# Kernel tuning notes

Hardware: AMD Instinct MI355X
Metric: run time of the kernel (lower is better)

Reference implementation:

```python
import jax, jax.numpy as jnp
import numpy as np

RADIUS = 0.07          # gno_config.gno_radius
SCALES = (1.0, 2.0)    # gno_config.scales


def _kernel_mlp(pair, kW1, kb1, kW2, kb2, kW3, kb3):
    # ChannelMLP inside IntegralTransform: gelu between layers, none after last
    h = jax.nn.gelu(pair @ kW1 + kb1)
    h = jax.nn.gelu(h @ kW2 + kb2)
    return h @ kW3 + kb3


def setup_inputs() -> dict:
    key = jax.random.key(0)
    ks = jax.random.split(key, 8)
    B, N, NL, CD, IN_C, C, H = 2, 2048, 512, 2, 16, 32, 32

    def glorot(k, shape):
        return jax.random.normal(k, shape) / jnp.sqrt(jnp.float32(shape[0]))

    return {
        "x_coord": jax.random.uniform(ks[0], (B, N, CD), dtype=jnp.float32),
        "pndata": jax.random.normal(ks[1], (B, N, IN_C), dtype=jnp.float32),
        "latent_tokens_coord": jax.random.uniform(ks[2], (NL, CD), dtype=jnp.float32),
        # lifting ChannelMLP (n_layers=1 -> single 1x1 conv == linear)
        "W_lift": glorot(ks[3], (IN_C, C)),
        "b_lift": jnp.zeros((C,), jnp.float32),
        # kernel MLP: [2*coord_dim=4] -> 32 -> 32 -> out_channels=32
        "kW1": glorot(ks[4], (2 * CD, H)),
        "kb1": jnp.zeros((H,), jnp.float32),
        "kW2": glorot(ks[5], (H, H)),
        "kb2": jnp.zeros((H,), jnp.float32),
        "kW3": glorot(ks[6], (H, C)),
        "kb3": jnp.zeros((C,), jnp.float32),
    }


def reference(x_coord, pndata, latent_tokens_coord,
              W_lift, b_lift, kW1, kb1, kW2, kb2, kW3, kb3):
    # lifting: [B,N,in_c] -> [B,N,C]
    f = pndata @ W_lift + b_lift

    B, N, CD = x_coord.shape
    NL = latent_tokens_coord.shape[0]

    y = x_coord[:, None, :, :]                      # [B,1,N,CD] source coords
    xq = latent_tokens_coord[None, :, None, :]      # [1,NL,1,CD] query coords
    # kernel input = cat(y_j, x_i) per (query i, source j) pair -> [B,NL,N,2*CD]
    pair = jnp.concatenate([jnp.broadcast_to(y, (B, NL, N, CD)),
                            jnp.broadcast_to(xq, (B, NL, N, CD))], axis=-1)
    kvals = _kernel_mlp(pair, kW1, kb1, kW2, kb2, kW3, kb3)  # [B,NL,N,C]

    d2 = jnp.sum((y - xq) ** 2, axis=-1)            # [B,NL,N] squared distances

    out = jnp.zeros((B, NL, kvals.shape[-1]), f.dtype)
    for s in SCALES:  # fixed small set of scales (2)
        # radius neighbor search expressed as dense mask (faithful to ball query)
        mask = (d2 <= (RADIUS * s) ** 2).astype(f.dtype)      # [B,NL,N]
        cnt = jnp.maximum(jnp.sum(mask, axis=-1), 1.0)        # [B,NL]
        # 'linear' transform: mean_j k(x_i,y_j) * f(y_j) over neighbors
        agg = jnp.einsum('bijc,bjc,bij->bic', kvals, f, mask)
        out = out + agg / cnt[..., None]
    return out  # [B,NL,C]
```

## Files before the change

kernel.cpp:

```cpp
#include <hip/hip_runtime.h>

static constexpr int B_ = 2, N_ = 2048, NL_ = 512, IN_C_ = 16, C_ = 32, H_ = 32;
static constexpr float R1SQ = (float)(0.07 * 0.07);
static constexpr float R2SQ = (float)(0.14 * 0.14);

typedef __attribute__((ext_vector_type(8))) short bf16x8;
typedef __attribute__((ext_vector_type(4))) float f32x4;

__device__ __forceinline__ float gelu_tanh(float x) {
    float z2 = 2.0f * 0.7978845608028654f * x * fmaf(0.044715f * x, x, 1.0f);
    float e = __expf(z2);
    return x * (1.0f - 1.0f / (e + 1.0f));
}

__device__ __forceinline__ short f2bf(float x) {
    unsigned u = __float_as_uint(x);
    u += 0x7fffu + ((u >> 16) & 1u);
    return (short)(u >> 16);
}

__global__ __launch_bounds__(128)
void magno_fused(const float* __restrict__ x_coord,
                 const float* __restrict__ lat,
                 const float* __restrict__ kW1, const float* __restrict__ kb1,
                 const float* __restrict__ kW2, const float* __restrict__ kb2,
                 const float* __restrict__ kW3, const float* __restrict__ kb3,
                 const float* __restrict__ pnd,
                 const float* __restrict__ Wl,
                 const float* __restrict__ bl,
                 float* __restrict__ out)
{
    __shared__ float sR0[H_], sR1[H_], sA1[H_];
    __shared__ unsigned jlist[N_];
    __shared__ __align__(16) short strans[2][64 * 40];
    __shared__ float sred[2][C_];
    __shared__ int s_n, s_c1;

    const int tid  = threadIdx.x;
    const int lane = tid & 63;
    const int wid  = tid >> 6;
    const int qd   = lane >> 4;
    const int li   = lane & 15;
    const int bi = blockIdx.x;
    const int b = bi >> 9, i = bi & (NL_ - 1);
    const float xq0 = lat[2 * i], xq1 = lat[2 * i + 1];

    if (tid == 0) { s_n = 0; s_c1 = 0; }
    if (tid < H_) {
        sR0[tid] = kW1[tid];
        sR1[tid] = kW1[H_ + tid];
        sA1[tid] = fmaf(xq0, kW1[2 * H_ + tid], fmaf(xq1, kW1[3 * H_ + tid], kb1[tid]));
    }

    bf16x8 w2f[2], w3f[2], wlf[2];
#pragma unroll
    for (int nt = 0; nt < 2; ++nt) {
        int n0 = li + 16 * nt;
#pragma unroll
        for (int jj = 0; jj < 8; ++jj) {
            int k = qd * 8 + jj;
            w2f[nt][jj] = f2bf(kW2[k * H_ + n0]);
            w3f[nt][jj] = f2bf(kW3[k * C_ + n0]);
            wlf[nt][jj] = (k < IN_C_) ? f2bf(Wl[k * C_ + n0]) : (short)0;
        }
    }
    const float b2A = kb2[li], b2B = kb2[li + 16];
    const float b3A = kb3[li], b3B = kb3[li + 16];
    const float blA = bl[li],  blB = bl[li + 16];
    __syncthreads();

    const float2* __restrict__ xc = (const float2*)(x_coord + (size_t)b * N_ * 2);
    const unsigned long long ltmask = (1ull << lane) - 1ull;
    for (int j0 = tid; j0 < N_; j0 += 128) {
        float2 y = xc[j0];
        float dy0 = y.x - xq0, dy1 = y.y - xq1;
        float d2 = dy0 * dy0 + dy1 * dy1;
        bool in2 = d2 <= R2SQ;
        bool in1 = d2 <= R1SQ;
        unsigned long long m2 = __ballot(in2);
        unsigned long long m1 = __ballot(in1);
        int basew = 0;
        if (lane == 0) {
            basew = atomicAdd(&s_n, __popcll(m2));
            atomicAdd(&s_c1, __popcll(m1));
        }
        basew = __shfl(basew, 0, 64);
        if (in2) {
            int pos = basew + __popcll(m2 & ltmask);
            jlist[pos] = (unsigned)j0 | (in1 ? 0x80000000u : 0u);
        }
    }
    __syncthreads();
    const int n = s_n;
    const float inv2 = 1.0f / (float)(n > 0 ? n : 1);
    const float inv1 = 1.0f / (float)(s_c1 > 0 ? s_c1 : 1);

    float r0v[8], r1v[8], a1v[8];
#pragma unroll
    for (int jj = 0; jj < 8; ++jj) {
        int k = qd * 8 + jj;
        r0v[jj] = sR0[k]; r1v[jj] = sR1[k]; a1v[jj] = sA1[k];
    }

    const float* __restrict__ pbase = pnd + (size_t)b * N_ * IN_C_;
    short* tb = &strans[wid][0];

    float accA = 0.0f, accB = 0.0f;
    const int nIter = (n + 127) >> 7;

    for (int it = 0; it < nIter; ++it) {
        const int base = it * 128 + 64 * wid;

        bf16x8 hfrag[4], paf[4];
#pragma unroll
        for (int mt = 0; mt < 4; ++mt) {
            int e = base + 16 * mt + li;
            unsigned pk = jlist[e < N_ ? e : 0];
            int j = (int)(pk & (unsigned)(N_ - 1));
            float2 y = xc[j];
#pragma unroll
            for (int jj = 0; jj < 8; ++jj)
                hfrag[mt][jj] = f2bf(gelu_tanh(fmaf(y.x, r0v[jj], fmaf(y.y, r1v[jj], a1v[jj]))));
            if (qd < 2) {
                const float4* p4 = (const float4*)(pbase + (size_t)j * IN_C_ + qd * 8);
                float4 v0 = p4[0], v1 = p4[1];
                paf[mt][0] = f2bf(v0.x); paf[mt][1] = f2bf(v0.y);
                paf[mt][2] = f2bf(v0.z); paf[mt][3] = f2bf(v0.w);
                paf[mt][4] = f2bf(v1.x); paf[mt][5] = f2bf(v1.y);
                paf[mt][6] = f2bf(v1.z); paf[mt][7] = f2bf(v1.w);
            } else {
#pragma unroll
                for (int jj = 0; jj < 8; ++jj) paf[mt][jj] = (short)0;
            }
        }

        f32x4 accF[4][2], acc2[4][2];
#pragma unroll
        for (int mt = 0; mt < 4; ++mt)
#pragma unroll
            for (int nt = 0; nt < 2; ++nt) {
                f32x4 z = {0.f, 0.f, 0.f, 0.f};
                accF[mt][nt] = __builtin_amdgcn_mfma_f32_16x16x32_bf16(paf[mt],   wlf[nt], z, 0, 0, 0);
                acc2[mt][nt] = __builtin_amdgcn_mfma_f32_16x16x32_bf16(hfrag[mt], w2f[nt], z, 0, 0, 0);
            }

#pragma unroll
        for (int mt = 0; mt < 4; ++mt)
#pragma unroll
            for (int nt = 0; nt < 2; ++nt) {
                float bb = nt ? b2B : b2A;
                int hid = li + 16 * nt;
#pragma unroll
                for (int r = 0; r < 4; ++r) {
                    int entry = 16 * mt + 4 * qd + r;
                    tb[entry * 40 + hid] = f2bf(gelu_tanh(acc2[mt][nt][r] + bb));
                }
            }
        __syncthreads();

        bf16x8 h2f[4];
#pragma unroll
        for (int mt = 0; mt < 4; ++mt)
            h2f[mt] = *(const bf16x8*)&tb[(li + 16 * mt) * 40 + qd * 8];
        __syncthreads();

        f32x4 acc3[4][2];
#pragma unroll
        for (int mt = 0; mt < 4; ++mt)
#pragma unroll
            for (int nt = 0; nt < 2; ++nt) {
                f32x4 z = {0.f, 0.f, 0.f, 0.f};
                acc3[mt][nt] = __builtin_amdgcn_mfma_f32_16x16x32_bf16(h2f[mt], w3f[nt], z, 0, 0, 0);
            }

#pragma unroll
        for (int mt = 0; mt < 4; ++mt)
#pragma unroll
            for (int r = 0; r < 4; ++r) {
                int e = base + 16 * mt + 4 * qd + r;
                unsigned pk = jlist[e < N_ ? e : 0];
                float w = (e < n) ? (inv2 + ((pk & 0x80000000u) ? inv1 : 0.0f)) : 0.0f;
                float fA = accF[mt][0][r] + blA;
                float fB = accF[mt][1][r] + blB;
                accA = fmaf(w * fA, acc3[mt][0][r] + b3A, accA);
                accB = fmaf(w * fB, acc3[mt][1][r] + b3B, accB);
            }
    }

    accA += __shfl_xor(accA, 16, 64);
    accA += __shfl_xor(accA, 32, 64);
    accB += __shfl_xor(accB, 16, 64);
    accB += __shfl_xor(accB, 32, 64);
    if (lane < 16) {
        sred[wid][li] = accA;
        sred[wid][li + 16] = accB;
    }
    __syncthreads();
    if (tid < C_) out[(size_t)bi * C_ + tid] = sred[0][tid] + sred[1][tid];
}

extern "C" void kernel_launch(void* const* d_in, const int* in_sizes, int n_in,
                              void* d_out, int out_size, void* d_ws, size_t ws_size,
                              hipStream_t stream) {
    const float* x_coord = (const float*)d_in[0];
    const float* pndata  = (const float*)d_in[1];
    const float* lat     = (const float*)d_in[2];
    const float* W_lift  = (const float*)d_in[3];
    const float* b_lift  = (const float*)d_in[4];
    const float* kW1     = (const float*)d_in[5];
    const float* kb1     = (const float*)d_in[6];
    const float* kW2     = (const float*)d_in[7];
    const float* kb2     = (const float*)d_in[8];
    const float* kW3     = (const float*)d_in[9];
    const float* kb3     = (const float*)d_in[10];
    float* out = (float*)d_out;

    magno_fused<<<B_ * NL_, 128, 0, stream>>>(
        x_coord, lat, kW1, kb1, kW2, kb2, kW3, kb3,
        pndata, W_lift, b_lift, out);
}
```

Measured before the change: 101.4 us.

## Precompute lifted features in separate kernel and widen blocks to four waves

Splits the lifting linear layer into its own kernel that writes f to workspace, so the main kernel no longer recomputes the lift via an extra MFMA per neighbor for every query. The main kernel moves to 256 threads (4 waves), preloads coordinates for the neighbor search in unrolled form, and skips inactive waves when the neighbor count is small. It adds a second launch and gathers fp32 f rows from global memory, and f now stays in fp32 instead of bf16. Larger blocks may leave waves idle when neighbor lists are short.

```diff
diff --git a/kernel.cpp b/kernel.cpp
--- a/kernel.cpp
+++ b/kernel.cpp
@@ -19,21 +19,40 @@
     return (short)(u >> 16);
 }
 
-__global__ __launch_bounds__(128)
-void magno_fused(const float* __restrict__ x_coord,
-                 const float* __restrict__ lat,
-                 const float* __restrict__ kW1, const float* __restrict__ kb1,
-                 const float* __restrict__ kW2, const float* __restrict__ kb2,
-                 const float* __restrict__ kW3, const float* __restrict__ kb3,
-                 const float* __restrict__ pnd,
-                 const float* __restrict__ Wl,
-                 const float* __restrict__ bl,
-                 float* __restrict__ out)
+__global__ __launch_bounds__(256)
+void lift_kernel(const float* __restrict__ pnd,
+                 const float* __restrict__ Wl, const float* __restrict__ bl,
+                 float* __restrict__ f)
+{
+    __shared__ float sW[IN_C_ * C_];
+    __shared__ float sb[C_];
+    int tid = threadIdx.x;
+    for (int idx = tid; idx < IN_C_ * C_; idx += 256) sW[idx] = Wl[idx];
+    if (tid < C_) sb[tid] = bl[tid];
+    __syncthreads();
+    int c = tid & 31;
+    int row = blockIdx.x * 8 + (tid >> 5);
+    if (row >= B_ * N_) return;
+    const float* p = pnd + (size_t)row * IN_C_;
+    float s = sb[c];
+#pragma unroll
+    for (int m = 0; m < IN_C_; ++m) s = fmaf(p[m], sW[m * C_ + c], s);
+    f[(size_t)row * C_ + c] = s;
+}
+
+__global__ __launch_bounds__(256)
+void magno_mfma(const float* __restrict__ x_coord,
+                const float* __restrict__ lat,
+                const float* __restrict__ kW1, const float* __restrict__ kb1,
+                const float* __restrict__ kW2, const float* __restrict__ kb2,
+                const float* __restrict__ kW3, const float* __restrict__ kb3,
+                const float* __restrict__ f,
+                float* __restrict__ out)
 {
     __shared__ float sR0[H_], sR1[H_], sA1[H_];
     __shared__ unsigned jlist[N_];
-    __shared__ __align__(16) short strans[2][64 * 40];
-    __shared__ float sred[2][C_];
+    __shared__ __align__(16) short strans[4][64 * 40];
+    __shared__ float sred[4][C_];
     __shared__ int s_n, s_c1;
 
     const int tid  = threadIdx.x;
@@ -45,35 +64,36 @@
     const int b = bi >> 9, i = bi & (NL_ - 1);
     const float xq0 = lat[2 * i], xq1 = lat[2 * i + 1];
 
+    bf16x8 w2f[2], w3f[2];
+#pragma unroll
+    for (int nt = 0; nt < 2; ++nt) {
+        int n0 = li + 16 * nt;
+#pragma unroll
+        for (int jj = 0; jj < 8; ++jj) {
+            int k = qd * 8 + jj;
+            w2f[nt][jj] = f2bf(kW2[k * H_ + n0]);
+            w3f[nt][jj] = f2bf(kW3[k * C_ + n0]);
+        }
+    }
+    const float b2A = kb2[li], b2B = kb2[li + 16];
+    const float b3A = kb3[li], b3B = kb3[li + 16];
+
     if (tid == 0) { s_n = 0; s_c1 = 0; }
     if (tid < H_) {
         sR0[tid] = kW1[tid];
         sR1[tid] = kW1[H_ + tid];
         sA1[tid] = fmaf(xq0, kW1[2 * H_ + tid], fmaf(xq1, kW1[3 * H_ + tid], kb1[tid]));
     }
-
-    bf16x8 w2f[2], w3f[2], wlf[2];
-#pragma unroll
-    for (int nt = 0; nt < 2; ++nt) {
-        int n0 = li + 16 * nt;
-#pragma unroll
-        for (int jj = 0; jj < 8; ++jj) {
-            int k = qd * 8 + jj;
-            w2f[nt][jj] = f2bf(kW2[k * H_ + n0]);
-            w3f[nt][jj] = f2bf(kW3[k * C_ + n0]);
-            wlf[nt][jj] = (k < IN_C_) ? f2bf(Wl[k * C_ + n0]) : (short)0;
-        }
-    }
-    const float b2A = kb2[li], b2B = kb2[li + 16];
-    const float b3A = kb3[li], b3B = kb3[li + 16];
-    const float blA = bl[li],  blB = bl[li + 16];
     __syncthreads();
 
     const float2* __restrict__ xc = (const float2*)(x_coord + (size_t)b * N_ * 2);
     const unsigned long long ltmask = (1ull << lane) - 1ull;
-    for (int j0 = tid; j0 < N_; j0 += 128) {
-        float2 y = xc[j0];
-        float dy0 = y.x - xq0, dy1 = y.y - xq1;
+    float2 ys[8];
+#pragma unroll
+    for (int t = 0; t < 8; ++t) ys[t] = xc[tid + 256 * t];
+#pragma unroll
+    for (int t = 0; t < 8; ++t) {
+        float dy0 = ys[t].x - xq0, dy1 = ys[t].y - xq1;
         float d2 = dy0 * dy0 + dy1 * dy1;
         bool in2 = d2 <= R2SQ;
         bool in1 = d2 <= R1SQ;
@@ -87,7 +107,7 @@
         basew = __shfl(basew, 0, 64);
         if (in2) {
             int pos = basew + __popcll(m2 & ltmask);
-            jlist[pos] = (unsigned)j0 | (in1 ? 0x80000000u : 0u);
+            jlist[pos] = (unsigned)(tid + 256 * t) | (in1 ? 0x80000000u : 0u);
         }
     }
     __syncthreads();
@@ -102,89 +122,81 @@
         r0v[jj] = sR0[k]; r1v[jj] = sR1[k]; a1v[jj] = sA1[k];
     }
 
-    const float* __restrict__ pbase = pnd + (size_t)b * N_ * IN_C_;
     short* tb = &strans[wid][0];
+    const float* __restrict__ fbase = f + (size_t)b * N_ * C_;
 
     float accA = 0.0f, accB = 0.0f;
-    const int nIter = (n + 127) >> 7;
+    const int nIter = (n + 255) >> 8;
 
     for (int it = 0; it < nIter; ++it) {
-        const int base = it * 128 + 64 * wid;
-
-        bf16x8 hfrag[4], paf[4];
-#pragma unroll
-        for (int mt = 0; mt < 4; ++mt) {
-            int e = base + 16 * mt + li;
-            unsigned pk = jlist[e < N_ ? e : 0];
-            int j = (int)(pk & (unsigned)(N_ - 1));
-            float2 y = xc[j];
-#pragma unroll
-            for (int jj = 0; jj < 8; ++jj)
-                hfrag[mt][jj] = f2bf(gelu_tanh(fmaf(y.x, r0v[jj], fmaf(y.y, r1v[jj], a1v[jj]))));
-            if (qd < 2) {
-                const float4* p4 = (const float4*)(pbase + (size_t)j * IN_C_ + qd * 8);
-                float4 v0 = p4[0], v1 = p4[1];
-                paf[mt][0] = f2bf(v0.x); paf[mt][1] = f2bf(v0.y);
-                paf[mt][2] = f2bf(v0.z); paf[mt][3] = f2bf(v0.w);
-                paf[mt][4] = f2bf(v1.x); paf[mt][5] = f2bf(v1.y);
-                paf[mt][6] = f2bf(v1.z); paf[mt][7] = f2bf(v1.w);
-            } else {
-#pragma unroll
-                for (int jj = 0; jj < 8; ++jj) paf[mt][jj] = (short)0;
+        const int base = it * 256 + 64 * wid;
+        const bool active = (base < n);
+
+        bf16x8 h2f[4];
+        f32x4 accF_unused;
+        f32x4 acc2[4][2];
+        if (active) {
+            bf16x8 hfrag[4];
+#pragma unroll
+            for (int mt = 0; mt < 4; ++mt) {
+                int e = base + 16 * mt + li;
+                unsigned pk = jlist[e < N_ ? e : 0];
+                int j = (int)(pk & (unsigned)(N_ - 1));
+                float2 y = xc[j];
+#pragma unroll
+                for (int jj = 0; jj < 8; ++jj)
+                    hfrag[mt][jj] = f2bf(gelu_tanh(fmaf(y.x, r0v[jj], fmaf(y.y, r1v[jj], a1v[jj]))));
             }
-        }
-
-        f32x4 accF[4][2], acc2[4][2];
-#pragma unroll
-        for (int mt = 0; mt < 4; ++mt)
-#pragma unroll
-            for (int nt = 0; nt < 2; ++nt) {
-                f32x4 z = {0.f, 0.f, 0.f, 0.f};
-                accF[mt][nt] = __builtin_amdgcn_mfma_f32_16x16x32_bf16(paf[mt],   wlf[nt], z, 0, 0, 0);
-                acc2[mt][nt] = __builtin_amdgcn_mfma_f32_16x16x32_bf16(hfrag[mt], w2f[nt], z, 0, 0, 0);
-            }
-
-#pragma unroll
-        for (int mt = 0; mt < 4; ++mt)
-#pragma unroll
-            for (int nt = 0; nt < 2; ++nt) {
-                float bb = nt ? b2B : b2A;
-                int hid = li + 16 * nt;
+#pragma unroll
+            for (int mt = 0; mt < 4; ++mt)
+#pragma unroll
+                for (int nt = 0; nt < 2; ++nt) {
+                    f32x4 z = {0.f, 0.f, 0.f, 0.f};
+                    acc2[mt][nt] = __builtin_amdgcn_mfma_f32_16x16x32_bf16(hfrag[mt], w2f[nt], z, 0, 0, 0);
+                }
+#pragma unroll
+            for (int mt = 0; mt < 4; ++mt)
+#pragma unroll
+                for (int nt = 0; nt < 2; ++nt) {
+                    float bb = nt ? b2B : b2A;
+                    int hid = li + 16 * nt;
+#pragma unroll
+                    for (int r = 0; r < 4; ++r) {
+                        int entry = 16 * mt + 4 * qd + r;
+                        tb[entry * 40 + hid] = f2bf(gelu_tanh(acc2[mt][nt][r] + bb));
+                    }
+                }
+        }
+        __syncthreads();
+        if (active) {
+#pragma unroll
+            for (int mt = 0; mt < 4; ++mt)
+                h2f[mt] = *(const bf16x8*)&tb[(li + 16 * mt) * 40 + qd * 8];
+        }
+        __syncthreads();
+        if (active) {
+            f32x4 acc3[4][2];
+#pragma unroll
+            for (int mt = 0; mt < 4; ++mt)
+#pragma unroll
+                for (int nt = 0; nt < 2; ++nt) {
+                    f32x4 z = {0.f, 0.f, 0.f, 0.f};
+                    acc3[mt][nt] = __builtin_amdgcn_mfma_f32_16x16x32_bf16(h2f[mt], w3f[nt], z, 0, 0, 0);
+                }
+#pragma unroll
+            for (int mt = 0; mt < 4; ++mt)
 #pragma unroll
                 for (int r = 0; r < 4; ++r) {
-                    int entry = 16 * mt + 4 * qd + r;
-                    tb[entry * 40 + hid] = f2bf(gelu_tanh(acc2[mt][nt][r] + bb));
-                }
-            }
-        __syncthreads();
-
-        bf16x8 h2f[4];
-#pragma unroll
-        for (int mt = 0; mt < 4; ++mt)
-            h2f[mt] = *(const bf16x8*)&tb[(li + 16 * mt) * 40 + qd * 8];
-        __syncthreads();
-
-        f32x4 acc3[4][2];
-#pragma unroll
-        for (int mt = 0; mt < 4; ++mt)
-#pragma unroll
-            for (int nt = 0; nt < 2; ++nt) {
-                f32x4 z = {0.f, 0.f, 0.f, 0.f};
-                acc3[mt][nt] = __builtin_amdgcn_mfma_f32_16x16x32_bf16(h2f[mt], w3f[nt], z, 0, 0, 0);
-            }
-
-#pragma unroll
-        for (int mt = 0; mt < 4; ++mt)
-#pragma unroll
-            for (int r = 0; r < 4; ++r) {
-                int e = base + 16 * mt + 4 * qd + r;
-                unsigned pk = jlist[e < N_ ? e : 0];
-                float w = (e < n) ? (inv2 + ((pk & 0x80000000u) ? inv1 : 0.0f)) : 0.0f;
-                float fA = accF[mt][0][r] + blA;
-                float fB = accF[mt][1][r] + blB;
-                accA = fmaf(w * fA, acc3[mt][0][r] + b3A, accA);
-                accB = fmaf(w * fB, acc3[mt][1][r] + b3B, accB);
-            }
+                    int e = base + 16 * mt + 4 * qd + r;
+                    unsigned pk = jlist[e < N_ ? e : 0];
+                    int j = (int)(pk & (unsigned)(N_ - 1));
+                    float w = (e < n) ? (inv2 + ((pk & 0x80000000u) ? inv1 : 0.0f)) : 0.0f;
+                    const float* fr = fbase + (size_t)j * C_;
+                    float fA = fr[li], fB = fr[li + 16];
+                    accA = fmaf(w * fA, acc3[mt][0][r] + b3A, accA);
+                    accB = fmaf(w * fB, acc3[mt][1][r] + b3B, accB);
+                }
+        }
     }
 
     accA += __shfl_xor(accA, 16, 64);
@@ -196,7 +208,8 @@
         sred[wid][li + 16] = accB;
     }
     __syncthreads();
-    if (tid < C_) out[(size_t)bi * C_ + tid] = sred[0][tid] + sred[1][tid];
+    if (tid < C_)
+        out[(size_t)bi * C_ + tid] = (sred[0][tid] + sred[1][tid]) + (sred[2][tid] + sred[3][tid]);
 }
 
 extern "C" void kernel_launch(void* const* d_in, const int* in_sizes, int n_in,
@@ -215,7 +228,8 @@
     const float* kb3     = (const float*)d_in[10];
     float* out = (float*)d_out;
 
-    magno_fused<<<B_ * NL_, 128, 0, stream>>>(
-        x_coord, lat, kW1, kb1, kW2, kb2, kW3, kb3,
-        pndata, W_lift, b_lift, out);
-}
+    float* f = (float*)d_ws;
+    lift_kernel<<<(B_ * N_ + 7) / 8, 256, 0, stream>>>(pndata, W_lift, b_lift, f);
+    magno_mfma<<<B_ * NL_, 256, 0, stream>>>(
+        x_coord, lat, kW1, kb1, kW2, kb2, kW3, kb3, f, out);
+}
```

Measured after the change: 95.12 us. 6.2% less time.
